# Performance work log

Hardware: AMD Instinct MI355X
Metric: run time of the kernel (lower is better)

Reference implementation:

```python
import jax, jax.numpy as jnp
import numpy as np
import math

T, D, DFF, E = 4096, 1024, 2048, 8
DEPTH_RATIO = 2.0 / 4.0  # layer_idx / n_layers
P_INIT = 0.3


def setup_inputs() -> dict:
    key = jax.random.key(0)
    ks = jax.random.split(key, 6)
    bias_init = -math.log(1.0 / P_INIT - 1.0)  # logit(0.3)
    return {
        "x": jax.random.normal(ks[0], (T, D), dtype=jnp.float32),
        "W_probe": jax.random.normal(ks[1], (E, D), dtype=jnp.float32) * 0.05,
        "b_probe": jnp.full((E,), bias_init, dtype=jnp.float32),
        "W_up": jax.random.normal(ks[2], (E, DFF, D), dtype=jnp.float32) * (1.0 / math.sqrt(D)),
        "W_gate": jax.random.normal(ks[3], (E, DFF, D), dtype=jnp.float32) * (1.0 / math.sqrt(D)),
        "W_down": jax.random.normal(ks[4], (E, D, DFF), dtype=jnp.float32) * (1.0 / math.sqrt(DFF)),
        "tau_base": jnp.full((1,), bias_init, dtype=jnp.float32),
        "gamma": jnp.full((1,), 0.5, dtype=jnp.float32),
        "w_depth": jnp.full((1,), 2.0, dtype=jnp.float32),
    }


def reference(x, W_probe, b_probe, W_up, W_gate, W_down, tau_base, gamma, w_depth):
    # DepthThreshold: tau_l = tau_base + gamma * silu(w_depth * (l/L))  (logit space)
    tau = tau_base[0] + gamma[0] * jax.nn.silu(w_depth[0] * DEPTH_RATIO)
    # MicroProbe: per-expert D->1 projections -> logits [T, E]
    logits = x @ W_probe.T + b_probe
    confidence = jax.nn.sigmoid(logits)            # [T, E]
    active = (logits > tau).astype(x.dtype)        # hard routing mask [T, E]
    scale = confidence * active                    # combine weight per (token, expert)
    # sparse_expert_dispatch, SwiGLU experts (dense-equivalent math):
    up = jnp.einsum('td,efd->etf', x, W_up)        # [E, T, DFF]
    gate = jnp.einsum('td,efd->etf', x, W_gate)    # [E, T, DFF]
    h = up * jax.nn.silu(gate)                     # [E, T, DFF]
    down = jnp.einsum('etf,edf->etd', h, W_down)   # [E, T, D]
    out = jnp.einsum('etd,te->td', down, scale)    # scatter-combine over experts
    return out
```

## Files before the change

kernel.cpp:

```cpp
#include <hip/hip_runtime.h>
#include <hip/hip_bf16.h>

#define T_DIM 4096
#define D_DIM 1024
#define DFF   2048
#define E_NUM 8

typedef short short8 __attribute__((ext_vector_type(8)));
typedef float f32x4  __attribute__((ext_vector_type(4)));

__device__ __forceinline__ unsigned short f2bf(float f) {
  union { float f; unsigned u; } v; v.f = f;
  unsigned r = v.u + 0x7FFFu + ((v.u >> 16) & 1u);
  return (unsigned short)(r >> 16);
}

__device__ __forceinline__ float bf2f(unsigned short b) {
  union { unsigned u; float f; } v; v.u = ((unsigned)b) << 16; return v.f;
}

__device__ __forceinline__ void load_lds16(const unsigned short* g, unsigned short* l) {
  __builtin_amdgcn_global_load_lds((const __attribute__((address_space(1))) void*)g,
                                   (__attribute__((address_space(3))) void*)l, 16, 0, 0);
}

__global__ void probe_kernel(const float* __restrict__ x, const float* __restrict__ Wp,
                             const float* __restrict__ bp, const float* __restrict__ tb,
                             const float* __restrict__ gm, const float* __restrict__ wdp,
                             float* __restrict__ scale) {
  int wave = threadIdx.x >> 6;
  int lane = threadIdx.x & 63;
  int t = blockIdx.x * 4 + wave;
  const float4* xr = (const float4*)(x + (size_t)t * D_DIM);
  float4 a[4];
#pragma unroll
  for (int k = 0; k < 4; k++) a[k] = xr[k * 64 + lane];
  float z = wdp[0] * 0.5f;
  float tau = tb[0] + gm[0] * (z / (1.f + expf(-z)));
#pragma unroll
  for (int e = 0; e < E_NUM; e++) {
    const float4* wr = (const float4*)(Wp + (size_t)e * D_DIM);
    float acc = 0.f;
#pragma unroll
    for (int k = 0; k < 4; k++) {
      float4 b = wr[k * 64 + lane];
      acc += a[k].x * b.x + a[k].y * b.y + a[k].z * b.z + a[k].w * b.w;
    }
#pragma unroll
    for (int off = 32; off > 0; off >>= 1) acc += __shfl_down(acc, off);
    if (lane == 0) {
      float logit = acc + bp[e];
      scale[t * E_NUM + e] = (logit > tau) ? (1.f / (1.f + expf(-logit))) : 0.f;
    }
  }
}

__global__ void compact_kernel(const float* __restrict__ scale, int* __restrict__ idxb,
                               float* __restrict__ scsb, int* __restrict__ cntb,
                               int* __restrict__ slotOfb) {
  int e = blockIdx.x;
  for (int t = threadIdx.x; t < T_DIM; t += 256) {
    float s = scale[t * E_NUM + e];
    if (s > 0.f) {
      int slot = atomicAdd(&cntb[e], 1);
      idxb[e * T_DIM + slot] = t;
      scsb[e * T_DIM + slot] = s;
      slotOfb[e * T_DIM + t] = slot;
    }
  }
}

__global__ void cvt_kernel(const float* __restrict__ src, unsigned short* __restrict__ dst) {
  int i = blockIdx.x * 256 + threadIdx.x;
  float4 v = ((const float4*)src)[i];
  ushort4 o;
  o.x = f2bf(v.x); o.y = f2bf(v.y); o.z = f2bf(v.z); o.w = f2bf(v.w);
  ((ushort4*)dst)[i] = o;
}

__global__ void cvt_w_kernel(const float* __restrict__ wu, const float* __restrict__ wg,
                             const float* __restrict__ wdn,
                             unsigned short* __restrict__ ou, unsigned short* __restrict__ og,
                             unsigned short* __restrict__ od) {
  int m = blockIdx.y;
  size_t i = (size_t)blockIdx.x * 256 + threadIdx.x;
  const float* s = (m == 0) ? wu : (m == 1) ? wg : wdn;
  unsigned short* d = (m == 0) ? ou : (m == 1) ? og : od;
  float4 v = ((const float4*)s)[i];
  ushort4 o;
  o.x = f2bf(v.x); o.y = f2bf(v.y); o.z = f2bf(v.z); o.w = f2bf(v.w);
  ((ushort4*)d)[i] = o;
}

__global__ void cvt3_kernel(const float* __restrict__ wu, const float* __restrict__ wg,
                            const float* __restrict__ wdn,
                            unsigned short* __restrict__ ou, unsigned short* __restrict__ og,
                            unsigned short* __restrict__ od) {
  int b = blockIdx.x;
  int m = b >> 11;
  int i = (b & 2047) * 256 + threadIdx.x;
  const float* s = (m == 0) ? wu : (m == 1) ? wg : wdn;
  unsigned short* d = (m == 0) ? ou : (m == 1) ? og : od;
  float4 v = ((const float4*)s)[i];
  ushort4 o;
  o.x = f2bf(v.x); o.y = f2bf(v.y); o.z = f2bf(v.z); o.w = f2bf(v.w);
  ((ushort4*)d)[i] = o;
}

__global__ void __launch_bounds__(256, 2)
upgate_kernel(const unsigned short* __restrict__ A,
              const unsigned short* __restrict__ Bu_base,
              const unsigned short* __restrict__ Bg_base,
              size_t wstride, size_t hstride,
              const int* __restrict__ idxb, const float* __restrict__ scsb,
              const int* __restrict__ cntb, int e_base,
              unsigned short* __restrict__ H_base) {
  int x, y, z;
  if (gridDim.y == 1) {
    int wid = blockIdx.x;
    z = wid & 7;
    int i = wid >> 3;
    x = i & 31;
    y = i >> 5;
  } else {
    x = blockIdx.x; y = blockIdx.y; z = blockIdx.z;
  }
  const int e = e_base + z;
  const int rowA0 = x * 128;
  if (rowA0 >= cntb[e]) return;
  __shared__ unsigned short smem[3 * 12288];
  const unsigned short* Bu = Bu_base + (size_t)z * wstride;
  const unsigned short* Bg = Bg_base + (size_t)z * wstride;
  unsigned short* H = H_base + (size_t)z * hstride;
  const int tid = threadIdx.x;
  const int wave = tid >> 6, lane = tid & 63;
  const int quad = lane >> 4, l15 = lane & 15;
  const int wm = (wave >> 1) * 64, wn = (wave & 1) * 64;
  const int rowB0 = y * 128;

  f32x4 accU[4][4], accG[4][4];
#pragma unroll
  for (int i2 = 0; i2 < 4; i2++)
#pragma unroll
    for (int j = 0; j < 4; j++) {
      accU[i2][j] = (f32x4){0.f, 0.f, 0.f, 0.f};
      accG[i2][j] = (f32x4){0.f, 0.f, 0.f, 0.f};
    }

  const int j0 = tid, j1 = tid + 256;
  const int ar0 = rowA0 + (j0 >> 2), ar1 = rowA0 + (j1 >> 2);
  const int br0 = rowB0 + (j0 >> 2), br1 = rowB0 + (j1 >> 2);
  const int c0 = (j0 & 3) * 8, c1 = (j1 & 3) * 8;
  const int ta0 = idxb[e * T_DIM + ar0];
  const int ta1 = idxb[e * T_DIM + ar1];

#define UG_STAGE(buf, kk) do {                                                 \
    unsigned short* _b = smem + (buf) * 12288;                                 \
    load_lds16(A  + (size_t)ta0 * D_DIM + (kk) + c0, _b + j0 * 8);             \
    load_lds16(A  + (size_t)ta1 * D_DIM + (kk) + c1, _b + j1 * 8);             \
    load_lds16(Bu + (size_t)br0 * D_DIM + (kk) + c0, _b + 4096 + j0 * 8);      \
    load_lds16(Bu + (size_t)br1 * D_DIM + (kk) + c1, _b + 4096 + j1 * 8);      \
    load_lds16(Bg + (size_t)br0 * D_DIM + (kk) + c0, _b + 8192 + j0 * 8);      \
    load_lds16(Bg + (size_t)br1 * D_DIM + (kk) + c1, _b + 8192 + j1 * 8);      \
  } while (0)

  UG_STAGE(0, 0);
  UG_STAGE(1, 32);
  for (int ks = 0; ks < 32; ks++) {
    if (ks < 30) {
      UG_STAGE((ks + 2) % 3, (ks + 2) * 32);
      asm volatile("s_waitcnt vmcnt(12)" ::: "memory");
    } else if (ks == 30) {
      asm volatile("s_waitcnt vmcnt(6)" ::: "memory");
    } else {
      asm volatile("s_waitcnt vmcnt(0)" ::: "memory");
    }
    __builtin_amdgcn_sched_barrier(0);
    __builtin_amdgcn_s_barrier();
    __builtin_amdgcn_sched_barrier(0);

    unsigned short* sA = smem + (ks % 3) * 12288;
    unsigned short* sU = sA + 4096;
    unsigned short* sG = sA + 8192;
    short8 af[4], bu[4], bg[4];
#pragma unroll
    for (int mt = 0; mt < 4; mt++)
      af[mt] = *(const short8*)(sA + (wm + mt * 16 + l15) * 32 + quad * 8);
#pragma unroll
    for (int nt = 0; nt < 4; nt++) {
      bu[nt] = *(const short8*)(sU + (wn + nt * 16 + l15) * 32 + quad * 8);
      bg[nt] = *(const short8*)(sG + (wn + nt * 16 + l15) * 32 + quad * 8);
    }
#pragma unroll
    for (int mt = 0; mt < 4; mt++)
#pragma unroll
      for (int nt = 0; nt < 4; nt++) {
        accU[mt][nt] = __builtin_amdgcn_mfma_f32_16x16x32_bf16(af[mt], bu[nt], accU[mt][nt], 0, 0, 0);
        accG[mt][nt] = __builtin_amdgcn_mfma_f32_16x16x32_bf16(af[mt], bg[nt], accG[mt][nt], 0, 0, 0);
      }
    asm volatile("s_waitcnt lgkmcnt(0)" ::: "memory");
    __builtin_amdgcn_sched_barrier(0);
    __builtin_amdgcn_s_barrier();
    __builtin_amdgcn_sched_barrier(0);
  }
#undef UG_STAGE

#pragma unroll
  for (int mt = 0; mt < 4; mt++) {
#pragma unroll
    for (int r = 0; r < 4; r++) {
      int row = rowA0 + wm + mt * 16 + quad * 4 + r;
      float s = scsb[e * T_DIM + row];
#pragma unroll
      for (int nt = 0; nt < 4; nt++) {
        int col = rowB0 + wn + nt * 16 + l15;
        float u = accU[mt][nt][r];
        float g = accG[mt][nt][r];
        float h = s * u * (g / (1.f + __expf(-g)));
        H[(size_t)row * DFF + col] = f2bf(h);
      }
    }
  }
}

__global__ void __launch_bounds__(256, 2)
down_slots_kernel(const unsigned short* __restrict__ hb,
                  const unsigned short* __restrict__ wdb,
                  const int* __restrict__ cntb,
                  unsigned short* __restrict__ de) {
  int wid = blockIdx.x;
  const int e = wid & 7;
  int i = wid >> 3;
  const int x = i & 31;
  const int y = i >> 5;
  const int rowA0 = x * 128;
  if (rowA0 >= cntb[e]) return;
  const size_t HSZ = (size_t)T_DIM * DFF;
  const size_t WSZ = (size_t)D_DIM * DFF;
  __shared__ unsigned short smem[3 * 8192];
  const unsigned short* A = hb + (size_t)e * HSZ;
  const unsigned short* B = wdb + (size_t)e * WSZ;
  const int tid = threadIdx.x;
  const int wave = tid >> 6, lane = tid & 63;
  const int quad = lane >> 4, l15 = lane & 15;
  const int wm = (wave >> 1) * 64, wn = (wave & 1) * 64;
  const int rowB0 = y * 128;

  f32x4 acc[4][4];
#pragma unroll
  for (int i2 = 0; i2 < 4; i2++)
#pragma unroll
    for (int j = 0; j < 4; j++) acc[i2][j] = (f32x4){0.f, 0.f, 0.f, 0.f};

  const int j0 = tid, j1 = tid + 256;
  const int ar0 = rowA0 + (j0 >> 2), ar1 = rowA0 + (j1 >> 2);
  const int br0 = rowB0 + (j0 >> 2), br1 = rowB0 + (j1 >> 2);
  const int c0 = (j0 & 3) * 8, c1 = (j1 & 3) * 8;

#define DS_STAGE(buf, kk) do {                                                  \
    unsigned short* _b = smem + (buf) * 8192;                                   \
    load_lds16(A + (size_t)ar0 * DFF + (kk) + c0, _b + j0 * 8);                 \
    load_lds16(A + (size_t)ar1 * DFF + (kk) + c1, _b + j1 * 8);                 \
    load_lds16(B + (size_t)br0 * DFF + (kk) + c0, _b + 4096 + j0 * 8);          \
    load_lds16(B + (size_t)br1 * DFF + (kk) + c1, _b + 4096 + j1 * 8);          \
  } while (0)

  DS_STAGE(0, 0);
  DS_STAGE(1, 32);
  for (int ks = 0; ks < 64; ks++) {
    if (ks < 62) {
      DS_STAGE((ks + 2) % 3, (ks + 2) * 32);
      asm volatile("s_waitcnt vmcnt(8)" ::: "memory");
    } else if (ks == 62) {
      asm volatile("s_waitcnt vmcnt(4)" ::: "memory");
    } else {
      asm volatile("s_waitcnt vmcnt(0)" ::: "memory");
    }
    __builtin_amdgcn_sched_barrier(0);
    __builtin_amdgcn_s_barrier();
    __builtin_amdgcn_sched_barrier(0);

    unsigned short* sA = smem + (ks % 3) * 8192;
    unsigned short* sB = sA + 4096;
    short8 af[4], bf[4];
#pragma unroll
    for (int mt = 0; mt < 4; mt++)
      af[mt] = *(const short8*)(sA + (wm + mt * 16 + l15) * 32 + quad * 8);
#pragma unroll
    for (int nt = 0; nt < 4; nt++)
      bf[nt] = *(const short8*)(sB + (wn + nt * 16 + l15) * 32 + quad * 8);
#pragma unroll
    for (int mt = 0; mt < 4; mt++)
#pragma unroll
      for (int nt = 0; nt < 4; nt++)
        acc[mt][nt] = __builtin_amdgcn_mfma_f32_16x16x32_bf16(af[mt], bf[nt], acc[mt][nt], 0, 0, 0);
    asm volatile("s_waitcnt lgkmcnt(0)" ::: "memory");
    __builtin_amdgcn_sched_barrier(0);
    __builtin_amdgcn_s_barrier();
    __builtin_amdgcn_sched_barrier(0);
  }
#undef DS_STAGE

#pragma unroll
  for (int mt = 0; mt < 4; mt++) {
#pragma unroll
    for (int r = 0; r < 4; r++) {
      int row = rowA0 + wm + mt * 16 + quad * 4 + r;
#pragma unroll
      for (int nt = 0; nt < 4; nt++) {
        int col = rowB0 + wn + nt * 16 + l15;
        de[((size_t)e * T_DIM + row) * D_DIM + col] = f2bf(acc[mt][nt][r]);
      }
    }
  }
}

__global__ void combine_kernel(const unsigned short* __restrict__ de,
                               const int* __restrict__ slotOfb,
                               float* __restrict__ out) {
  int t = blockIdx.x;
  int d4 = threadIdx.x;
  float4 acc = {0.f, 0.f, 0.f, 0.f};
#pragma unroll
  for (int e = 0; e < E_NUM; e++) {
    int s = slotOfb[e * T_DIM + t];
    if (s >= 0) {
      ushort4 v = ((const ushort4*)(de + ((size_t)e * T_DIM + s) * D_DIM))[d4];
      acc.x += bf2f(v.x); acc.y += bf2f(v.y); acc.z += bf2f(v.z); acc.w += bf2f(v.w);
    }
  }
  ((float4*)(out + (size_t)t * D_DIM))[d4] = acc;
}

__global__ void __launch_bounds__(256, 2)
down_kernel(const unsigned short* __restrict__ A_base,
            const unsigned short* __restrict__ B_base,
            size_t hstride, size_t wstride,
            const int* __restrict__ idxb, const int* __restrict__ cntb, int e_base,
            float* __restrict__ out) {
  const int e = e_base + blockIdx.z;
  const int rowA0 = blockIdx.x * 128;
  if (rowA0 >= cntb[e]) return;
  __shared__ unsigned short smem[2 * 128 * 32];
  unsigned short* sA = smem;
  unsigned short* sB = smem + 4096;
  const unsigned short* A = A_base + (size_t)blockIdx.z * hstride;
  const unsigned short* B = B_base + (size_t)blockIdx.z * wstride;
  const int tid = threadIdx.x;
  const int wave = tid >> 6, lane = tid & 63;
  const int quad = lane >> 4, l15 = lane & 15;
  const int wm = (wave >> 1) * 64, wn = (wave & 1) * 64;
  const int rowB0 = blockIdx.y * 128;

  f32x4 acc[4][4];
#pragma unroll
  for (int i = 0; i < 4; i++)
#pragma unroll
    for (int j = 0; j < 4; j++) acc[i][j] = (f32x4){0.f, 0.f, 0.f, 0.f};

  const int j0 = tid, j1 = tid + 256;
  const int ar0 = rowA0 + (j0 >> 2), ar1 = rowA0 + (j1 >> 2);
  const int br0 = rowB0 + (j0 >> 2), br1 = rowB0 + (j1 >> 2);
  const int c0 = (j0 & 3) * 8, c1 = (j1 & 3) * 8;

  for (int k0 = 0; k0 < DFF; k0 += 32) {
    __syncthreads();
    load_lds16(A + (size_t)ar0 * DFF + k0 + c0, sA + j0 * 8);
    load_lds16(A + (size_t)ar1 * DFF + k0 + c1, sA + j1 * 8);
    load_lds16(B + (size_t)br0 * DFF + k0 + c0, sB + j0 * 8);
    load_lds16(B + (size_t)br1 * DFF + k0 + c1, sB + j1 * 8);
    __syncthreads();

    short8 af[4], bf[4];
#pragma unroll
    for (int mt = 0; mt < 4; mt++)
      af[mt] = *(const short8*)(sA + (wm + mt * 16 + l15) * 32 + quad * 8);
#pragma unroll
    for (int nt = 0; nt < 4; nt++)
      bf[nt] = *(const short8*)(sB + (wn + nt * 16 + l15) * 32 + quad * 8);
#pragma unroll
    for (int mt = 0; mt < 4; mt++)
#pragma unroll
      for (int nt = 0; nt < 4; nt++)
        acc[mt][nt] = __builtin_amdgcn_mfma_f32_16x16x32_bf16(af[mt], bf[nt], acc[mt][nt], 0, 0, 0);
  }

#pragma unroll
  for (int mt = 0; mt < 4; mt++) {
#pragma unroll
    for (int r = 0; r < 4; r++) {
      int row = rowA0 + wm + mt * 16 + quad * 4 + r;
      int tok = idxb[e * T_DIM + row];
#pragma unroll
      for (int nt = 0; nt < 4; nt++) {
        int col = rowB0 + wn + nt * 16 + l15;
        atomicAdd(&out[(size_t)tok * D_DIM + col], acc[mt][nt][r]);
      }
    }
  }
}

extern "C" void kernel_launch(void* const* d_in, const int* in_sizes, int n_in,
                              void* d_out, int out_size, void* d_ws, size_t ws_size,
                              hipStream_t stream) {
  const float* x   = (const float*)d_in[0];
  const float* Wp  = (const float*)d_in[1];
  const float* bp  = (const float*)d_in[2];
  const float* Wu  = (const float*)d_in[3];
  const float* Wg  = (const float*)d_in[4];
  const float* Wd  = (const float*)d_in[5];
  const float* tb  = (const float*)d_in[6];
  const float* gm  = (const float*)d_in[7];
  const float* wdp = (const float*)d_in[8];
  float* out = (float*)d_out;

  const size_t WSZ = (size_t)DFF * D_DIM;
  const size_t HSZ = (size_t)T_DIM * DFF;

  char* ws = (char*)d_ws;
  float* scale         = (float*)ws;
  int*   idxb          = (int*)(ws + 131072);
  float* scsb          = (float*)(ws + 262144);
  int*   slotOfb       = (int*)(ws + 393216);
  int*   cntb          = (int*)(ws + 524288);
  unsigned short* xb   = (unsigned short*)(ws + 536576);
  const size_t HEAD    = 536576;

  hipMemsetAsync(ws + 131072, 0, 262144, stream);
  hipMemsetAsync(ws + 393216, 0xFF, 131072, stream);
  hipMemsetAsync(ws + 524288, 0, 4096, stream);
  probe_kernel<<<T_DIM / 4, 256, 0, stream>>>(x, Wp, bp, tb, gm, wdp, scale);
  compact_kernel<<<E_NUM, 256, 0, stream>>>(scale, idxb, scsb, cntb, slotOfb);
  cvt_kernel<<<T_DIM * D_DIM / 1024, 256, 0, stream>>>(x, xb);

  const size_t FULL_REQ = HEAD + 8388608 + 3 * (WSZ * 2) * E_NUM + HSZ * 2 * E_NUM;
  if (ws_size >= FULL_REQ) {
    unsigned short* wub = xb + (size_t)T_DIM * D_DIM;
    unsigned short* wgb = wub + WSZ * E_NUM;
    unsigned short* wdb = wgb + WSZ * E_NUM;
    unsigned short* hb  = wdb + WSZ * E_NUM;

    dim3 gc(WSZ * E_NUM / 1024, 3);
    cvt_w_kernel<<<gc, 256, 0, stream>>>(Wu, Wg, Wd, wub, wgb, wdb);

    upgate_kernel<<<dim3(4096, 1, 1), 256, 0, stream>>>(xb, wub, wgb, WSZ, HSZ,
                                                        idxb, scsb, cntb, 0, hb);
    unsigned short* de = wub;
    down_slots_kernel<<<dim3(2048, 1, 1), 256, 0, stream>>>(hb, wdb, cntb, de);
    combine_kernel<<<dim3(T_DIM, 1, 1), 256, 0, stream>>>(de, slotOfb, out);
  } else {
    hipMemsetAsync(out, 0, (size_t)T_DIM * D_DIM * sizeof(float), stream);
    unsigned short* wub = xb + (size_t)T_DIM * D_DIM;
    unsigned short* wgb = wub + WSZ;
    unsigned short* wdb = wgb + WSZ;
    unsigned short* hb  = wdb + WSZ;

    for (int e = 0; e < E_NUM; e++) {
      cvt3_kernel<<<3 * (DFF * D_DIM / 1024), 256, 0, stream>>>(
          Wu + e * WSZ, Wg + e * WSZ, Wd + e * WSZ, wub, wgb, wdb);
      dim3 g1(T_DIM / 128, DFF / 128, 1);
      upgate_kernel<<<g1, 256, 0, stream>>>(xb, wub, wgb, 0, 0, idxb, scsb, cntb, e, hb);
      dim3 g2(T_DIM / 128, D_DIM / 128, 1);
      down_kernel<<<g2, 256, 0, stream>>>(hb, wdb, 0, 0, idxb, cntb, e, out);
    }
  }
}
```

Baseline: 472.9 us.

## Use larger 512-thread GEMM tiles with 4-stage single-barrier pipeline for experts

```diff
diff --git a/kernel.cpp b/kernel.cpp
--- a/kernel.cpp
+++ b/kernel.cpp
@@ -107,6 +107,222 @@
   ((ushort4*)d)[i] = o;
 }
 
+__global__ void __launch_bounds__(512, 1)
+upgate_big_kernel(const unsigned short* __restrict__ A,
+                  const unsigned short* __restrict__ Bu_base,
+                  const unsigned short* __restrict__ Bg_base,
+                  size_t wstride, size_t hstride,
+                  const int* __restrict__ idxb, const float* __restrict__ scsb,
+                  const int* __restrict__ cntb,
+                  unsigned short* __restrict__ H_base) {
+  int wid = blockIdx.x;
+  const int e = wid & 7;
+  int i = wid >> 3;
+  const int x = i & 15;
+  const int y = i >> 4;
+  const int rowA0 = x * 256;
+  if (rowA0 >= cntb[e]) return;
+  __shared__ unsigned short smem[4 * 16384];
+  const unsigned short* Bu = Bu_base + (size_t)e * wstride;
+  const unsigned short* Bg = Bg_base + (size_t)e * wstride;
+  unsigned short* H = H_base + (size_t)e * hstride;
+  const int tid = threadIdx.x;
+  const int wave = tid >> 6, lane = tid & 63;
+  const int quad = lane >> 4, l15 = lane & 15;
+  const int wm = (wave >> 2) * 128;
+  const int wn = (wave & 3) * 32;
+  const int rowB0 = y * 128;
+
+  f32x4 accU[8][2], accG[8][2];
+#pragma unroll
+  for (int m = 0; m < 8; m++)
+#pragma unroll
+    for (int n = 0; n < 2; n++) {
+      accU[m][n] = (f32x4){0.f, 0.f, 0.f, 0.f};
+      accG[m][n] = (f32x4){0.f, 0.f, 0.f, 0.f};
+    }
+
+  const int j0 = tid, j1 = tid + 512;
+  const int ar0 = rowA0 + (j0 >> 2), ar1 = rowA0 + (j1 >> 2);
+  const int cA0 = (j0 & 3) * 8, cA1 = (j1 & 3) * 8;
+  const int brB = rowB0 + (tid >> 2);
+  const int cB = (tid & 3) * 8;
+  const int ta0 = idxb[e * T_DIM + ar0];
+  const int ta1 = idxb[e * T_DIM + ar1];
+
+#define UG_STAGE(buf, kk) do {                                                  \
+    unsigned short* _b = smem + (buf) * 16384;                                  \
+    load_lds16(A  + (size_t)ta0 * D_DIM + (kk) + cA0, _b + j0 * 8);             \
+    load_lds16(A  + (size_t)ta1 * D_DIM + (kk) + cA1, _b + j1 * 8);             \
+    load_lds16(Bu + (size_t)brB * D_DIM + (kk) + cB, _b + 8192 + tid * 8);      \
+    load_lds16(Bg + (size_t)brB * D_DIM + (kk) + cB, _b + 12288 + tid * 8);     \
+  } while (0)
+
+  UG_STAGE(0, 0);
+  UG_STAGE(1, 32);
+  for (int ks = 0; ks < 32; ks++) {
+    if (ks < 30) {
+      UG_STAGE((ks + 2) & 3, (ks + 2) * 32);
+      asm volatile("s_waitcnt vmcnt(8)" ::: "memory");
+    } else if (ks == 30) {
+      asm volatile("s_waitcnt vmcnt(4)" ::: "memory");
+    } else {
+      asm volatile("s_waitcnt vmcnt(0)" ::: "memory");
+    }
+    asm volatile("s_waitcnt lgkmcnt(0)" ::: "memory");
+    __builtin_amdgcn_sched_barrier(0);
+    __builtin_amdgcn_s_barrier();
+    __builtin_amdgcn_sched_barrier(0);
+
+    unsigned short* sA = smem + (ks & 3) * 16384;
+    unsigned short* sU = sA + 8192;
+    unsigned short* sG = sA + 12288;
+    short8 af[8], bu[2], bg[2];
+#pragma unroll
+    for (int mt = 0; mt < 8; mt++)
+      af[mt] = *(const short8*)(sA + (wm + mt * 16 + l15) * 32 + quad * 8);
+#pragma unroll
+    for (int nt = 0; nt < 2; nt++) {
+      bu[nt] = *(const short8*)(sU + (wn + nt * 16 + l15) * 32 + quad * 8);
+      bg[nt] = *(const short8*)(sG + (wn + nt * 16 + l15) * 32 + quad * 8);
+    }
+#pragma unroll
+    for (int mt = 0; mt < 8; mt++)
+#pragma unroll
+      for (int nt = 0; nt < 2; nt++) {
+        accU[mt][nt] = __builtin_amdgcn_mfma_f32_16x16x32_bf16(af[mt], bu[nt], accU[mt][nt], 0, 0, 0);
+        accG[mt][nt] = __builtin_amdgcn_mfma_f32_16x16x32_bf16(af[mt], bg[nt], accG[mt][nt], 0, 0, 0);
+      }
+    __builtin_amdgcn_sched_barrier(0);
+  }
+#undef UG_STAGE
+
+#pragma unroll
+  for (int mt = 0; mt < 8; mt++) {
+#pragma unroll
+    for (int r = 0; r < 4; r++) {
+      int row = rowA0 + wm + mt * 16 + quad * 4 + r;
+      float s = scsb[e * T_DIM + row];
+#pragma unroll
+      for (int nt = 0; nt < 2; nt++) {
+        int col = rowB0 + wn + nt * 16 + l15;
+        float u = accU[mt][nt][r];
+        float g = accG[mt][nt][r];
+        float h = s * u * (g / (1.f + __expf(-g)));
+        H[(size_t)row * DFF + col] = f2bf(h);
+      }
+    }
+  }
+}
+
+__global__ void __launch_bounds__(512, 1)
+down_big_kernel(const unsigned short* __restrict__ hb,
+                const unsigned short* __restrict__ wdb,
+                const int* __restrict__ cntb,
+                unsigned short* __restrict__ de) {
+  int wid = blockIdx.x;
+  const int e = wid & 7;
+  int i = wid >> 3;
+  const int x = i & 15;
+  const int y = i >> 4;
+  const int rowA0 = x * 256;
+  if (rowA0 >= cntb[e]) return;
+  const size_t HSZ = (size_t)T_DIM * DFF;
+  const size_t WSZ = (size_t)D_DIM * DFF;
+  __shared__ unsigned short smem[4 * 16384];
+  const unsigned short* A = hb + (size_t)e * HSZ;
+  const unsigned short* B = wdb + (size_t)e * WSZ;
+  const int tid = threadIdx.x;
+  const int wave = tid >> 6, lane = tid & 63;
+  const int quad = lane >> 4, l15 = lane & 15;
+  const int wm = (wave >> 2) * 128;
+  const int wn = (wave & 3) * 64;
+  const int rowB0 = y * 256;
+
+  f32x4 acc[8][4];
+#pragma unroll
+  for (int m = 0; m < 8; m++)
+#pragma unroll
+    for (int n = 0; n < 4; n++) acc[m][n] = (f32x4){0.f, 0.f, 0.f, 0.f};
+
+  const int j0 = tid, j1 = tid + 512;
+  const int ar0 = rowA0 + (j0 >> 2), ar1 = rowA0 + (j1 >> 2);
+  const int br0 = rowB0 + (j0 >> 2), br1 = rowB0 + (j1 >> 2);
+  const int c0 = (j0 & 3) * 8, c1 = (j1 & 3) * 8;
+
+#define DS_STAGE(buf, kk) do {                                                  \
+    unsigned short* _b = smem + (buf) * 16384;                                  \
+    load_lds16(A + (size_t)ar0 * DFF + (kk) + c0, _b + j0 * 8);                 \
+    load_lds16(A + (size_t)ar1 * DFF + (kk) + c1, _b + j1 * 8);                 \
+    load_lds16(B + (size_t)br0 * DFF + (kk) + c0, _b + 8192 + j0 * 8);          \
+    load_lds16(B + (size_t)br1 * DFF + (kk) + c1, _b + 8192 + j1 * 8);          \
+  } while (0)
+
+  DS_STAGE(0, 0);
+  DS_STAGE(1, 32);
+  for (int ks = 0; ks < 64; ks++) {
+    if (ks < 62) {
+      DS_STAGE((ks + 2) & 3, (ks + 2) * 32);
+      asm volatile("s_waitcnt vmcnt(8)" ::: "memory");
+    } else if (ks == 62) {
+      asm volatile("s_waitcnt vmcnt(4)" ::: "memory");
+    } else {
+      asm volatile("s_waitcnt vmcnt(0)" ::: "memory");
+    }
+    asm volatile("s_waitcnt lgkmcnt(0)" ::: "memory");
+    __builtin_amdgcn_sched_barrier(0);
+    __builtin_amdgcn_s_barrier();
+    __builtin_amdgcn_sched_barrier(0);
+
+    unsigned short* sA = smem + (ks & 3) * 16384;
+    unsigned short* sB = sA + 8192;
+    short8 af[8], bf[4];
+#pragma unroll
+    for (int mt = 0; mt < 8; mt++)
+      af[mt] = *(const short8*)(sA + (wm + mt * 16 + l15) * 32 + quad * 8);
+#pragma unroll
+    for (int nt = 0; nt < 4; nt++)
+      bf[nt] = *(const short8*)(sB + (wn + nt * 16 + l15) * 32 + quad * 8);
+#pragma unroll
+    for (int mt = 0; mt < 8; mt++)
+#pragma unroll
+      for (int nt = 0; nt < 4; nt++)
+        acc[mt][nt] = __builtin_amdgcn_mfma_f32_16x16x32_bf16(af[mt], bf[nt], acc[mt][nt], 0, 0, 0);
+    __builtin_amdgcn_sched_barrier(0);
+  }
+#undef DS_STAGE
+
+#pragma unroll
+  for (int mt = 0; mt < 8; mt++) {
+#pragma unroll
+    for (int r = 0; r < 4; r++) {
+      int row = rowA0 + wm + mt * 16 + quad * 4 + r;
+#pragma unroll
+      for (int nt = 0; nt < 4; nt++) {
+        int col = rowB0 + wn + nt * 16 + l15;
+        de[((size_t)e * T_DIM + row) * D_DIM + col] = f2bf(acc[mt][nt][r]);
+      }
+    }
+  }
+}
+
+__global__ void combine_kernel(const unsigned short* __restrict__ de,
+                               const int* __restrict__ slotOfb,
+                               float* __restrict__ out) {
+  int t = blockIdx.x;
+  int d4 = threadIdx.x;
+  float4 acc = {0.f, 0.f, 0.f, 0.f};
+#pragma unroll
+  for (int e = 0; e < E_NUM; e++) {
+    int s = slotOfb[e * T_DIM + t];
+    if (s >= 0) {
+      ushort4 v = ((const ushort4*)(de + ((size_t)e * T_DIM + s) * D_DIM))[d4];
+      acc.x += bf2f(v.x); acc.y += bf2f(v.y); acc.z += bf2f(v.z); acc.w += bf2f(v.w);
+    }
+  }
+  ((float4*)(out + (size_t)t * D_DIM))[d4] = acc;
+}
+
 __global__ void __launch_bounds__(256, 2)
 upgate_kernel(const unsigned short* __restrict__ A,
               const unsigned short* __restrict__ Bu_base,
@@ -115,16 +331,7 @@
               const int* __restrict__ idxb, const float* __restrict__ scsb,
               const int* __restrict__ cntb, int e_base,
               unsigned short* __restrict__ H_base) {
-  int x, y, z;
-  if (gridDim.y == 1) {
-    int wid = blockIdx.x;
-    z = wid & 7;
-    int i = wid >> 3;
-    x = i & 31;
-    y = i >> 5;
-  } else {
-    x = blockIdx.x; y = blockIdx.y; z = blockIdx.z;
-  }
+  int x = blockIdx.x, y = blockIdx.y, z = blockIdx.z;
   const int e = e_base + z;
   const int rowA0 = x * 128;
   if (rowA0 >= cntb[e]) return;
@@ -154,7 +361,7 @@
   const int ta0 = idxb[e * T_DIM + ar0];
   const int ta1 = idxb[e * T_DIM + ar1];
 
-#define UG_STAGE(buf, kk) do {                                                 \
+#define UGF_STAGE(buf, kk) do {                                                \
     unsigned short* _b = smem + (buf) * 12288;                                 \
     load_lds16(A  + (size_t)ta0 * D_DIM + (kk) + c0, _b + j0 * 8);             \
     load_lds16(A  + (size_t)ta1 * D_DIM + (kk) + c1, _b + j1 * 8);             \
@@ -164,11 +371,11 @@
     load_lds16(Bg + (size_t)br1 * D_DIM + (kk) + c1, _b + 8192 + j1 * 8);      \
   } while (0)
 
-  UG_STAGE(0, 0);
-  UG_STAGE(1, 32);
+  UGF_STAGE(0, 0);
+  UGF_STAGE(1, 32);
   for (int ks = 0; ks < 32; ks++) {
     if (ks < 30) {
-      UG_STAGE((ks + 2) % 3, (ks + 2) * 32);
+      UGF_STAGE((ks + 2) % 3, (ks + 2) * 32);
       asm volatile("s_waitcnt vmcnt(12)" ::: "memory");
     } else if (ks == 30) {
       asm volatile("s_waitcnt vmcnt(6)" ::: "memory");
@@ -203,7 +410,7 @@
     __builtin_amdgcn_s_barrier();
     __builtin_amdgcn_sched_barrier(0);
   }
-#undef UG_STAGE
+#undef UGF_STAGE
 
 #pragma unroll
   for (int mt = 0; mt < 4; mt++) {
@@ -221,115 +428,6 @@
       }
     }
   }
-}
-
-__global__ void __launch_bounds__(256, 2)
-down_slots_kernel(const unsigned short* __restrict__ hb,
-                  const unsigned short* __restrict__ wdb,
-                  const int* __restrict__ cntb,
-                  unsigned short* __restrict__ de) {
-  int wid = blockIdx.x;
-  const int e = wid & 7;
-  int i = wid >> 3;
-  const int x = i & 31;
-  const int y = i >> 5;
-  const int rowA0 = x * 128;
-  if (rowA0 >= cntb[e]) return;
-  const size_t HSZ = (size_t)T_DIM * DFF;
-  const size_t WSZ = (size_t)D_DIM * DFF;
-  __shared__ unsigned short smem[3 * 8192];
-  const unsigned short* A = hb + (size_t)e * HSZ;
-  const unsigned short* B = wdb + (size_t)e * WSZ;
-  const int tid = threadIdx.x;
-  const int wave = tid >> 6, lane = tid & 63;
-  const int quad = lane >> 4, l15 = lane & 15;
-  const int wm = (wave >> 1) * 64, wn = (wave & 1) * 64;
-  const int rowB0 = y * 128;
-
-  f32x4 acc[4][4];
-#pragma unroll
-  for (int i2 = 0; i2 < 4; i2++)
-#pragma unroll
-    for (int j = 0; j < 4; j++) acc[i2][j] = (f32x4){0.f, 0.f, 0.f, 0.f};
-
-  const int j0 = tid, j1 = tid + 256;
-  const int ar0 = rowA0 + (j0 >> 2), ar1 = rowA0 + (j1 >> 2);
-  const int br0 = rowB0 + (j0 >> 2), br1 = rowB0 + (j1 >> 2);
-  const int c0 = (j0 & 3) * 8, c1 = (j1 & 3) * 8;
-
-#define DS_STAGE(buf, kk) do {                                                  \
-    unsigned short* _b = smem + (buf) * 8192;                                   \
-    load_lds16(A + (size_t)ar0 * DFF + (kk) + c0, _b + j0 * 8);                 \
-    load_lds16(A + (size_t)ar1 * DFF + (kk) + c1, _b + j1 * 8);                 \
-    load_lds16(B + (size_t)br0 * DFF + (kk) + c0, _b + 4096 + j0 * 8);          \
-    load_lds16(B + (size_t)br1 * DFF + (kk) + c1, _b + 4096 + j1 * 8);          \
-  } while (0)
-
-  DS_STAGE(0, 0);
-  DS_STAGE(1, 32);
-  for (int ks = 0; ks < 64; ks++) {
-    if (ks < 62) {
-      DS_STAGE((ks + 2) % 3, (ks + 2) * 32);
-      asm volatile("s_waitcnt vmcnt(8)" ::: "memory");
-    } else if (ks == 62) {
-      asm volatile("s_waitcnt vmcnt(4)" ::: "memory");
-    } else {
-      asm volatile("s_waitcnt vmcnt(0)" ::: "memory");
-    }
-    __builtin_amdgcn_sched_barrier(0);
-    __builtin_amdgcn_s_barrier();
-    __builtin_amdgcn_sched_barrier(0);
-
-    unsigned short* sA = smem + (ks % 3) * 8192;
-    unsigned short* sB = sA + 4096;
-    short8 af[4], bf[4];
-#pragma unroll
-    for (int mt = 0; mt < 4; mt++)
-      af[mt] = *(const short8*)(sA + (wm + mt * 16 + l15) * 32 + quad * 8);
-#pragma unroll
-    for (int nt = 0; nt < 4; nt++)
-      bf[nt] = *(const short8*)(sB + (wn + nt * 16 + l15) * 32 + quad * 8);
-#pragma unroll
-    for (int mt = 0; mt < 4; mt++)
-#pragma unroll
-      for (int nt = 0; nt < 4; nt++)
-        acc[mt][nt] = __builtin_amdgcn_mfma_f32_16x16x32_bf16(af[mt], bf[nt], acc[mt][nt], 0, 0, 0);
-    asm volatile("s_waitcnt lgkmcnt(0)" ::: "memory");
-    __builtin_amdgcn_sched_barrier(0);
-    __builtin_amdgcn_s_barrier();
-    __builtin_amdgcn_sched_barrier(0);
-  }
-#undef DS_STAGE
-
-#pragma unroll
-  for (int mt = 0; mt < 4; mt++) {
-#pragma unroll
-    for (int r = 0; r < 4; r++) {
-      int row = rowA0 + wm + mt * 16 + quad * 4 + r;
-#pragma unroll
-      for (int nt = 0; nt < 4; nt++) {
-        int col = rowB0 + wn + nt * 16 + l15;
-        de[((size_t)e * T_DIM + row) * D_DIM + col] = f2bf(acc[mt][nt][r]);
-      }
-    }
-  }
-}
-
-__global__ void combine_kernel(const unsigned short* __restrict__ de,
-                               const int* __restrict__ slotOfb,
-                               float* __restrict__ out) {
-  int t = blockIdx.x;
-  int d4 = threadIdx.x;
-  float4 acc = {0.f, 0.f, 0.f, 0.f};
-#pragma unroll
-  for (int e = 0; e < E_NUM; e++) {
-    int s = slotOfb[e * T_DIM + t];
-    if (s >= 0) {
-      ushort4 v = ((const ushort4*)(de + ((size_t)e * T_DIM + s) * D_DIM))[d4];
-      acc.x += bf2f(v.x); acc.y += bf2f(v.y); acc.z += bf2f(v.z); acc.w += bf2f(v.w);
-    }
-  }
-  ((float4*)(out + (size_t)t * D_DIM))[d4] = acc;
 }
 
 __global__ void __launch_bounds__(256, 2)
@@ -443,10 +541,10 @@
     dim3 gc(WSZ * E_NUM / 1024, 3);
     cvt_w_kernel<<<gc, 256, 0, stream>>>(Wu, Wg, Wd, wub, wgb, wdb);
 
-    upgate_kernel<<<dim3(4096, 1, 1), 256, 0, stream>>>(xb, wub, wgb, WSZ, HSZ,
-                                                        idxb, scsb, cntb, 0, hb);
+    upgate_big_kernel<<<dim3(2048, 1, 1), 512, 0, stream>>>(xb, wub, wgb, WSZ, HSZ,
+                                                            idxb, scsb, cntb, hb);
     unsigned short* de = wub;
-    down_slots_kernel<<<dim3(2048, 1, 1), 256, 0, stream>>>(hb, wdb, cntb, de);
+    down_big_kernel<<<dim3(512, 1, 1), 512, 0, stream>>>(hb, wdb, cntb, de);
     combine_kernel<<<dim3(T_DIM, 1, 1), 256, 0, stream>>>(de, slotOfb, out);
   } else {
     hipMemsetAsync(out, 0, (size_t)T_DIM * D_DIM * sizeof(float), stream);
```

Measured after the change: 460.5 us. -2.6%, faster.
